# Kernel optimization log

Hardware: AMD Instinct MI355X
Metric: run time of the kernel (lower is better)

Reference implementation:

```python
import jax, jax.numpy as jnp
import numpy as np

B = 131072
USER_N = 100000
ITEM_N = 20000
CONCEPT_N = 128
D_IN = 3
NB_MOD_MAX = 12
M = NB_MOD_MAX + 2  # nb_mod_max_plus_sent


def setup_inputs() -> dict:
    key = jax.random.key(0)
    ks = jax.random.split(key, 7)
    user_ids = jax.random.randint(ks[0], (B,), 0, USER_N)
    item_ids = jax.random.randint(ks[1], (B,), 0, ITEM_N)
    concept_ids = jax.random.randint(ks[2], (B,), 0, CONCEPT_N)
    users_emb_weight = jax.random.normal(ks[3], (USER_N, CONCEPT_N), dtype=jnp.float32)
    item_resp_weight = jax.random.normal(ks[4], (ITEM_N * M, D_IN), dtype=jnp.float32)
    W = jax.random.normal(ks[5], (CONCEPT_N, D_IN, CONCEPT_N), dtype=jnp.float32)
    # nb_modalities in [2, nb_mod_max]; mask[i, j] = 0 for j in [1, nb_modalities[i]], inf elsewhere
    nb_modalities = jax.random.randint(ks[6], (ITEM_N,), 2, NB_MOD_MAX + 1)
    cols = jnp.arange(M)[None, :]  # (1, M)
    valid = (cols >= 1) & (cols <= nb_modalities[:, None])
    mask = jnp.where(valid, 0.0, jnp.inf).astype(jnp.float32)  # (ITEM_N, M)
    return {
        "user_ids": user_ids,
        "item_ids": item_ids,
        "concept_ids": concept_ids,
        "users_emb_weight": users_emb_weight,
        "item_resp_weight": item_resp_weight,
        "W": W,
        "mask": mask,
        "nb_modalities": nb_modalities,
    }


def reference(user_ids, item_ids, concept_ids, users_emb_weight, item_resp_weight, W, mask, nb_modalities):
    # W_t: (B, d_in, C)
    W_t = W[concept_ids]
    # im_idx: (B, M) row indices into the item-response embedding table
    im_idx = item_ids[:, None] * M + jnp.arange(M)[None, :]
    im_emb_prime = item_resp_weight[im_idx]  # (B, M, d_in)
    # bmm: (B, M, d_in) x (B, d_in, C) -> (B, M, C)
    im_emb = jnp.einsum('bmd,bdc->bmc', im_emb_prime, W_t)
    u_emb = users_emb_weight[user_ids]  # (B, C)
    diff = u_emb[:, None, :] - im_emb
    p_uim = jnp.sum(diff * diff, axis=2)  # (B, M)
    idx = jnp.argmin(p_uim + mask[item_ids, :], axis=1)  # (B,)
    nb = nb_modalities[item_ids]
    # mod_to_resp: ((idx - 1) / (nb - 1)) + 1
    responses = (idx.astype(jnp.float32) - 1.0) / (nb.astype(jnp.float32) - 1.0) + 1.0
    return responses
```

## Files before the change

### kernel.cpp

```cpp
#include <hip/hip_runtime.h>
#include <math.h>

static constexpr int B_TOTAL = 131072;
static constexpr int M_MOD   = 14;
static constexpr int C_DIM   = 128;

__global__ __launch_bounds__(256) void impact_kernel(
    const int*   __restrict__ user_ids,
    const int*   __restrict__ item_ids,
    const int*   __restrict__ concept_ids,
    const float* __restrict__ users_emb,
    const float* __restrict__ item_resp,
    const float* __restrict__ W,
    const int*   __restrict__ nb_mod,
    float*       __restrict__ out)
{
    const int s = threadIdx.x & 15;
    const int b = blockIdx.x * 16 + (threadIdx.x >> 4);

    const int uid = user_ids[b];
    const int iid = item_ids[b];
    const int cid = concept_ids[b];
    const int nb  = nb_mod[iid];

    const float4* up = (const float4*)(users_emb + (size_t)uid * C_DIM);
    const float4 uA = up[s], uB = up[s + 16];
    const float4* wp = (const float4*)(W + (size_t)cid * 3 * C_DIM);
    const float4 w0a = wp[s],      w0b = wp[16 + s];
    const float4 w1a = wp[32 + s], w1b = wp[48 + s];
    const float4 w2a = wp[64 + s], w2b = wp[80 + s];

    float v0 = 0.f, v1 = 0.f, v2 = 0.f;
    float g00 = 0.f, g01 = 0.f, g02 = 0.f, g11 = 0.f, g12 = 0.f, g22 = 0.f;
#define COL(uc, a0, a1, a2)                                                    \
    do {                                                                       \
        v0  = fmaf((a0), (uc), v0);  v1  = fmaf((a1), (uc), v1);               \
        v2  = fmaf((a2), (uc), v2);                                            \
        g00 = fmaf((a0), (a0), g00); g01 = fmaf((a0), (a1), g01);              \
        g02 = fmaf((a0), (a2), g02); g11 = fmaf((a1), (a1), g11);              \
        g12 = fmaf((a1), (a2), g12); g22 = fmaf((a2), (a2), g22);              \
    } while (0)
    COL(uA.x, w0a.x, w1a.x, w2a.x);
    COL(uA.y, w0a.y, w1a.y, w2a.y);
    COL(uA.z, w0a.z, w1a.z, w2a.z);
    COL(uA.w, w0a.w, w1a.w, w2a.w);
    COL(uB.x, w0b.x, w1b.x, w2b.x);
    COL(uB.y, w0b.y, w1b.y, w2b.y);
    COL(uB.z, w0b.z, w1b.z, w2b.z);
    COL(uB.w, w0b.w, w1b.w, w2b.w);
#undef COL

#pragma unroll
    for (int off = 8; off; off >>= 1) {
        v0  += __shfl_xor(v0,  off, 64);
        v1  += __shfl_xor(v1,  off, 64);
        v2  += __shfl_xor(v2,  off, 64);
        g00 += __shfl_xor(g00, off, 64);
        g01 += __shfl_xor(g01, off, 64);
        g02 += __shfl_xor(g02, off, 64);
        g11 += __shfl_xor(g11, off, 64);
        g12 += __shfl_xor(g12, off, 64);
        g22 += __shfl_xor(g22, off, 64);
    }

    float m = INFINITY;
    if (s < 12 && (s + 1) <= nb) {
        const float* pj = item_resp + ((size_t)iid * M_MOD + (s + 1)) * 3;
        const float p0 = pj[0], p1 = pj[1], p2 = pj[2];
        const float dot = fmaf(p0, v0, fmaf(p1, v1, p2 * v2));
        float q = p0 * p0 * g00;
        q = fmaf(p1 * p1, g11, q);
        q = fmaf(p2 * p2, g22, q);
        q = fmaf(2.0f * p0 * p1, g01, q);
        q = fmaf(2.0f * p0 * p2, g02, q);
        q = fmaf(2.0f * p1 * p2, g12, q);
        m = fmaf(-2.0f, dot, q);
    }
    float bm = m;
#pragma unroll
    for (int off = 8; off; off >>= 1)
        bm = fminf(bm, __shfl_xor(bm, off, 64));
    const unsigned long long mask = __ballot(m == bm);
    if (s == 0) {
        const int group = (threadIdx.x >> 4) & 3;
        const unsigned slice = (unsigned)((mask >> (group * 16)) & 0xffffu);
        const int jm1 = __builtin_ctz(slice);
        out[b] = (float)jm1 / (float)(nb - 1) + 1.0f;
    }
}

extern "C" void kernel_launch(void* const* d_in, const int* in_sizes, int n_in,
                              void* d_out, int out_size, void* d_ws, size_t ws_size,
                              hipStream_t stream) {
    const int*   user_ids    = (const int*)d_in[0];
    const int*   item_ids    = (const int*)d_in[1];
    const int*   concept_ids = (const int*)d_in[2];
    const float* users_emb   = (const float*)d_in[3];
    const float* item_resp   = (const float*)d_in[4];
    const float* W           = (const float*)d_in[5];
    const int*   nb_mod      = (const int*)d_in[7];
    float*       out         = (float*)d_out;

    dim3 grid(B_TOTAL / 16), block(256);
    impact_kernel<<<grid, block, 0, stream>>>(user_ids, item_ids, concept_ids,
                                              users_emb, item_resp, W, nb_mod, out);
}
```

Measured before the change: 111.5 us.

## Precompute per-concept Gram matrices and use DPP row reductions

```diff
diff --git a/kernel.cpp b/kernel.cpp
--- a/kernel.cpp
+++ b/kernel.cpp
@@ -4,6 +4,56 @@
 static constexpr int B_TOTAL = 131072;
 static constexpr int M_MOD   = 14;
 static constexpr int C_DIM   = 128;
+
+template <int CTRL>
+__device__ __forceinline__ float dpp_mov(float x) {
+    return __int_as_float(__builtin_amdgcn_update_dpp(
+        0, __float_as_int(x), CTRL, 0xF, 0xF, true));
+}
+#define ROW_SUM(x)                                                             \
+    do {                                                                       \
+        x += dpp_mov<0x128>(x);                                 \
+        x += dpp_mov<0x124>(x);                                 \
+        x += dpp_mov<0x04E>(x);                \
+        x += dpp_mov<0x0B1>(x);                \
+    } while (0)
+#define ROW_MIN(x)                                                             \
+    do {                                                                       \
+        x = fminf(x, dpp_mov<0x128>(x));                                       \
+        x = fminf(x, dpp_mov<0x124>(x));                                       \
+        x = fminf(x, dpp_mov<0x04E>(x));                                       \
+        x = fminf(x, dpp_mov<0x0B1>(x));                                       \
+    } while (0)
+
+__global__ __launch_bounds__(64) void gram_kernel(
+    const float* __restrict__ W, float* __restrict__ g)
+{
+    const int c = blockIdx.x;
+    const int l = threadIdx.x;
+    const float2* wp = (const float2*)(W + (size_t)c * 3 * C_DIM);
+    const float2 a0 = wp[l], a1 = wp[64 + l], a2 = wp[128 + l];
+    float g00 = a0.x * a0.x + a0.y * a0.y;
+    float g01 = a0.x * a1.x + a0.y * a1.y;
+    float g02 = a0.x * a2.x + a0.y * a2.y;
+    float g11 = a1.x * a1.x + a1.y * a1.y;
+    float g12 = a1.x * a2.x + a1.y * a2.y;
+    float g22 = a2.x * a2.x + a2.y * a2.y;
+#pragma unroll
+    for (int off = 32; off; off >>= 1) {
+        g00 += __shfl_xor(g00, off, 64);
+        g01 += __shfl_xor(g01, off, 64);
+        g02 += __shfl_xor(g02, off, 64);
+        g11 += __shfl_xor(g11, off, 64);
+        g12 += __shfl_xor(g12, off, 64);
+        g22 += __shfl_xor(g22, off, 64);
+    }
+    if (l == 0) {
+        float* o = g + c * 8;
+        o[0] = g00; o[1] = g01; o[2] = g02;
+        o[3] = g11; o[4] = g12; o[5] = g22;
+        o[6] = 0.f; o[7] = 0.f;
+    }
+}
 
 __global__ __launch_bounds__(256) void impact_kernel(
     const int*   __restrict__ user_ids,
@@ -13,6 +63,7 @@
     const float* __restrict__ item_resp,
     const float* __restrict__ W,
     const int*   __restrict__ nb_mod,
+    const float* __restrict__ gram,
     float*       __restrict__ out)
 {
     const int s = threadIdx.x & 15;
@@ -29,16 +80,17 @@
     const float4 w0a = wp[s],      w0b = wp[16 + s];
     const float4 w1a = wp[32 + s], w1b = wp[48 + s];
     const float4 w2a = wp[64 + s], w2b = wp[80 + s];
+    const float4 gA = ((const float4*)(gram + cid * 8))[0];
+    const float4 gB = ((const float4*)(gram + cid * 8))[1];
+    const float* pj = item_resp + ((size_t)iid * M_MOD + (s < 12 ? s + 1 : 1)) * 3;
+    const float p0 = pj[0], p1 = pj[1], p2 = pj[2];
 
     float v0 = 0.f, v1 = 0.f, v2 = 0.f;
-    float g00 = 0.f, g01 = 0.f, g02 = 0.f, g11 = 0.f, g12 = 0.f, g22 = 0.f;
 #define COL(uc, a0, a1, a2)                                                    \
     do {                                                                       \
-        v0  = fmaf((a0), (uc), v0);  v1  = fmaf((a1), (uc), v1);               \
-        v2  = fmaf((a2), (uc), v2);                                            \
-        g00 = fmaf((a0), (a0), g00); g01 = fmaf((a0), (a1), g01);              \
-        g02 = fmaf((a0), (a2), g02); g11 = fmaf((a1), (a1), g11);              \
-        g12 = fmaf((a1), (a2), g12); g22 = fmaf((a2), (a2), g22);              \
+        v0 = fmaf((a0), (uc), v0);                                             \
+        v1 = fmaf((a1), (uc), v1);                                             \
+        v2 = fmaf((a2), (uc), v2);                                             \
     } while (0)
     COL(uA.x, w0a.x, w1a.x, w2a.x);
     COL(uA.y, w0a.y, w1a.y, w2a.y);
@@ -49,37 +101,23 @@
     COL(uB.z, w0b.z, w1b.z, w2b.z);
     COL(uB.w, w0b.w, w1b.w, w2b.w);
 #undef COL
-
-#pragma unroll
-    for (int off = 8; off; off >>= 1) {
-        v0  += __shfl_xor(v0,  off, 64);
-        v1  += __shfl_xor(v1,  off, 64);
-        v2  += __shfl_xor(v2,  off, 64);
-        g00 += __shfl_xor(g00, off, 64);
-        g01 += __shfl_xor(g01, off, 64);
-        g02 += __shfl_xor(g02, off, 64);
-        g11 += __shfl_xor(g11, off, 64);
-        g12 += __shfl_xor(g12, off, 64);
-        g22 += __shfl_xor(g22, off, 64);
-    }
+    ROW_SUM(v0);
+    ROW_SUM(v1);
+    ROW_SUM(v2);
 
     float m = INFINITY;
     if (s < 12 && (s + 1) <= nb) {
-        const float* pj = item_resp + ((size_t)iid * M_MOD + (s + 1)) * 3;
-        const float p0 = pj[0], p1 = pj[1], p2 = pj[2];
         const float dot = fmaf(p0, v0, fmaf(p1, v1, p2 * v2));
-        float q = p0 * p0 * g00;
-        q = fmaf(p1 * p1, g11, q);
-        q = fmaf(p2 * p2, g22, q);
-        q = fmaf(2.0f * p0 * p1, g01, q);
-        q = fmaf(2.0f * p0 * p2, g02, q);
-        q = fmaf(2.0f * p1 * p2, g12, q);
+        float q = p0 * p0 * gA.x;
+        q = fmaf(p1 * p1, gA.w, q);
+        q = fmaf(p2 * p2, gB.y, q);
+        q = fmaf(2.0f * p0 * p1, gA.y, q);
+        q = fmaf(2.0f * p0 * p2, gA.z, q);
+        q = fmaf(2.0f * p1 * p2, gB.x, q);
         m = fmaf(-2.0f, dot, q);
     }
     float bm = m;
-#pragma unroll
-    for (int off = 8; off; off >>= 1)
-        bm = fminf(bm, __shfl_xor(bm, off, 64));
+    ROW_MIN(bm);
     const unsigned long long mask = __ballot(m == bm);
     if (s == 0) {
         const int group = (threadIdx.x >> 4) & 3;
@@ -99,9 +137,11 @@
     const float* item_resp   = (const float*)d_in[4];
     const float* W           = (const float*)d_in[5];
     const int*   nb_mod      = (const int*)d_in[7];
+    float*       gram        = (float*)d_ws;
     float*       out         = (float*)d_out;
 
-    dim3 grid(B_TOTAL / 16), block(256);
-    impact_kernel<<<grid, block, 0, stream>>>(user_ids, item_ids, concept_ids,
-                                              users_emb, item_resp, W, nb_mod, out);
+    gram_kernel<<<dim3(128), dim3(64), 0, stream>>>(W, gram);
+    impact_kernel<<<dim3(B_TOTAL / 16), dim3(256), 0, stream>>>(
+        user_ids, item_ids, concept_ids, users_emb, item_resp, W, nb_mod,
+        gram, out);
 }
```

Result: no change. 113.7 us (+2.0%).
